# Kernel tuning notes

Hardware: AMD Instinct MI355X
Metric: run time of the kernel (lower is better)

## Reference

```python
import jax, jax.numpy as jnp
import numpy as np

N_HEADS = 16
COS_SIM_SCALE = 8.0  # lucidrains flash_cosine_sim_attention default temperature
RMS_EPS = 1e-6
ROPE_THETA = 10000.0


def _rms_norm(t, g):
    # RMSNorm over head dim with learnable gain (QKNorm)
    return t * jax.lax.rsqrt(jnp.mean(t * t, axis=-1, keepdims=True) + RMS_EPS) * g


def _rotate_half(x):
    d = x.shape[-1]
    return jnp.concatenate([-x[..., d // 2:], x[..., : d // 2]], axis=-1)


def _image_rope_cos_sin(n, d, dtype):
    # 2D axial RoPE: first half of head dim encodes row position, second half column.
    side = int(np.sqrt(n))
    assert side * side == n, 'ImageRoPE expects a square token grid'
    n_freq = d // 4
    freqs = 1.0 / (ROPE_THETA ** (jnp.arange(n_freq, dtype=jnp.float32) / n_freq))
    pos = jnp.arange(side, dtype=jnp.float32)
    grid_h = jnp.repeat(pos, side)   # (n,) row index
    grid_w = jnp.tile(pos, side)     # (n,) col index
    ang_h = grid_h[:, None] * freqs  # (n, d//4)
    ang_w = grid_w[:, None] * freqs  # (n, d//4)
    # rotate-half convention: angles for dims [0:d//2] paired with [d//2:d]
    ang = jnp.concatenate([ang_h, ang_w], axis=-1)          # (n, d//2)
    ang = jnp.concatenate([ang, ang], axis=-1)              # (n, d)
    return jnp.cos(ang).astype(dtype), jnp.sin(ang).astype(dtype)


def setup_inputs() -> dict:
    key = jax.random.key(0)
    ks = jax.random.split(key, 6)
    b, n, dm = 8, 1024, 1024
    h = N_HEADS
    d = dm // h
    s = 1.0 / np.sqrt(dm)
    return {
        'x': jax.random.normal(ks[0], (b, n, dm), dtype=jnp.float32),
        'w_qkv': jax.random.normal(ks[1], (dm, 3 * dm), dtype=jnp.float32) * s,
        'b_qkv': jnp.zeros((3 * dm,), dtype=jnp.float32),
        'q_gain': jnp.ones((d,), dtype=jnp.float32),
        'k_gain': jnp.ones((d,), dtype=jnp.float32),
        'w_out': jax.random.normal(ks[2], (dm, dm), dtype=jnp.float32) * s,
        'b_out': jnp.zeros((dm,), dtype=jnp.float32),
    }


def reference(x, w_qkv, b_qkv, q_gain, k_gain, w_out, b_out):
    b, n, dm = x.shape
    h = N_HEADS
    d = dm // h
    qkv = x @ w_qkv + b_qkv                       # (b, n, 3*dm)
    qkv = qkv.reshape(b, n, 3, h, d)
    qkv = jnp.transpose(qkv, (2, 0, 3, 1, 4))     # (3, b, h, n, d)
    q, k, v = qkv[0], qkv[1], qkv[2]
    # QK-norm (RMSNorm over head dim)
    q = _rms_norm(q, q_gain)
    k = _rms_norm(k, k_gain)
    # 2D image RoPE
    cos, sin = _image_rope_cos_sin(n, d, x.dtype)
    q = q * cos + _rotate_half(q) * sin
    k = k * cos + _rotate_half(k) * sin
    # cosine-sim attention: l2-normalize q,k, fixed scale, softmax, weighted sum
    q = q / jnp.linalg.norm(q, axis=-1, keepdims=True)
    k = k / jnp.linalg.norm(k, axis=-1, keepdims=True)
    scores = jnp.einsum('bhnd,bhmd->bhnm', q, k) * COS_SIM_SCALE
    attn = jax.nn.softmax(scores, axis=-1)
    o = jnp.einsum('bhnm,bhmd->bhnd', attn, v)    # (b, h, n, d)
    o = jnp.transpose(o, (0, 2, 1, 3)).reshape(b, n, dm)
    return o @ w_out + b_out
```

## Files before the change

### kernel.cpp

```cpp
#include <hip/hip_runtime.h>
#include <hip/hip_bf16.h>
#include <cstdint>

typedef __bf16 bf16;
typedef __bf16 bf16x8 __attribute__((ext_vector_type(8)));
typedef __bf16 bf16x4 __attribute__((ext_vector_type(4)));
typedef float f32x4 __attribute__((ext_vector_type(4)));

__device__ inline bf16x8 cvt8(const float* __restrict__ p) {
  float4 a = *(const float4*)p;
  float4 b = *(const float4*)(p + 4);
  bf16x8 r;
  r[0] = (bf16)a.x; r[1] = (bf16)a.y; r[2] = (bf16)a.z; r[3] = (bf16)a.w;
  r[4] = (bf16)b.x; r[5] = (bf16)b.y; r[6] = (bf16)b.z; r[7] = (bf16)b.w;
  return r;
}

__device__ inline void gl_lds16(const bf16* g, bf16* l) {
  auto gp = reinterpret_cast<const __attribute__((address_space(1))) uint32_t*>(
      reinterpret_cast<uintptr_t>(g));
  auto lp = reinterpret_cast<__attribute__((address_space(3))) uint32_t*>(
      reinterpret_cast<uintptr_t>(l));
  __builtin_amdgcn_global_load_lds(gp, lp, 16, 0, 0);
}

#define BAR() asm volatile("s_barrier" ::: "memory")

__global__ __launch_bounds__(256) void cast_k(const float* __restrict__ in,
                                              bf16* __restrict__ out) {
  long i = ((long)blockIdx.x * 256 + threadIdx.x) * 8;
  *(bf16x8*)(out + i) = cvt8(in + i);
}

__global__ __launch_bounds__(256) void transpose_cast_k(const float* __restrict__ in,
                                                        bf16* __restrict__ out,
                                                        int R, int C) {
  __shared__ bf16 T[32][33];
  int tc = blockIdx.x * 32, tr = blockIdx.y * 32;
  int c = threadIdx.x & 31, r8 = threadIdx.x >> 5;
#pragma unroll
  for (int i = 0; i < 4; i++) {
    int r = r8 + i * 8;
    T[r][c] = (bf16)in[(long)(tr + r) * C + tc + c];
  }
  __syncthreads();
#pragma unroll
  for (int i = 0; i < 4; i++) {
    int r = r8 + i * 8;
    out[(long)(tc + r) * R + tr + c] = T[c][r];
  }
}

__global__ __launch_bounds__(512, 2) void gemm256(const bf16* __restrict__ A,
                                                  const bf16* __restrict__ Bt,
                                                  const float* __restrict__ bias,
                                                  int K,
                                                  bf16* __restrict__ qb,
                                                  bf16* __restrict__ kb,
                                                  bf16* __restrict__ v4,
                                                  const float* __restrict__ qg,
                                                  const float* __restrict__ kg) {
  __shared__ __align__(16) bf16 As[2][16384];
  __shared__ __align__(16) bf16 Bs[2][16384];

  const int tid = threadIdx.x;
  const int lane = tid & 63;
  const int w = tid >> 6;
  const int quad = lane >> 4;
  const int l16 = lane & 15;
  const int wr = w >> 2;
  const int wc = w & 3;

  const int gx = gridDim.x;
  const int bid = blockIdx.y * gx + blockIdx.x;
  const int cpx = (gx * gridDim.y) >> 3;
  const int sw = (bid & 7) * cpx + (bid >> 3);
  const int n0 = (sw % gx) * 256;
  const int m0 = (sw / gx) * 256;

  int srow[2], scof[2];
#pragma unroll
  for (int l = 0; l < 2; l++) {
    int s = l * 512 + tid;
    srow[l] = s >> 3;
    scof[l] = ((s & 7) ^ ((s >> 3) & 7)) * 8;
  }
  const bf16* aB0 = A + (long)(m0 + srow[0]) * K + scof[0];
  const bf16* aB1 = A + (long)(m0 + srow[1]) * K + scof[1];
  const bf16* bB0 = Bt + (long)(n0 + srow[0]) * K + scof[0];
  const bf16* bB1 = Bt + (long)(n0 + srow[1]) * K + scof[1];

#define STAGE_A(tb, kt1, h)                                                        \
  {                                                                                \
    gl_lds16(aB0 + (long)(h)*128 * K + (long)(kt1)*64, &As[tb][(h)*8192 + w * 512]); \
    gl_lds16(aB1 + (long)(h)*128 * K + (long)(kt1)*64,                             \
             &As[tb][(h)*8192 + 4096 + w * 512]);                                  \
  }
#define STAGE_B(tb, kt1, h)                                                        \
  {                                                                                \
    gl_lds16(bB0 + (long)(h)*128 * K + (long)(kt1)*64, &Bs[tb][(h)*8192 + w * 512]); \
    gl_lds16(bB1 + (long)(h)*128 * K + (long)(kt1)*64,                             \
             &Bs[tb][(h)*8192 + 4096 + w * 512]);                                  \
  }

  const int cq0 = ((quad) ^ (l16 & 7)) * 8;
  const int cq1 = ((4 + quad) ^ (l16 & 7)) * 8;
  const int aoff = wr * 8192 + l16 * 64;
  const int boff = wc * 4096 + l16 * 64;

  f32x4 acc[8][4];
#pragma unroll
  for (int i = 0; i < 8; i++)
#pragma unroll
    for (int j = 0; j < 4; j++) acc[i][j] = f32x4{0.f, 0.f, 0.f, 0.f};

#define MM16(MLO, AF, BF)                                                         \
  __builtin_amdgcn_s_setprio(1);                                                  \
  _Pragma("unroll") for (int mm = 0; mm < 4; mm++)                                \
      _Pragma("unroll") for (int nn = 0; nn < 4; nn++) acc[(MLO) + mm][nn] =      \
          __builtin_amdgcn_mfma_f32_16x16x32_bf16(AF[mm], BF[nn],                 \
                                                  acc[(MLO) + mm][nn], 0, 0, 0);  \
  __builtin_amdgcn_s_setprio(0);

  const int NK = K >> 6;
  STAGE_A(0, 0, 0); STAGE_A(0, 0, 1); STAGE_B(0, 0, 0); STAGE_B(0, 0, 1);

  for (int kt = 0; kt < NK; ++kt) {
    const int pb = kt & 1;
    const int tb = pb ^ 1;
    const bool pf = (kt + 1 < NK);
    bf16x8 afr[4], bfr[4];
    if (pf) {
      STAGE_A(tb, kt + 1, 0);
      STAGE_A(tb, kt + 1, 1);
      STAGE_B(tb, kt + 1, 0);
      STAGE_B(tb, kt + 1, 1);
      asm volatile("s_waitcnt vmcnt(8)" ::: "memory");
    } else {
      asm volatile("s_waitcnt vmcnt(0)" ::: "memory");
    }
    BAR();
#pragma unroll
    for (int n = 0; n < 4; n++) bfr[n] = *(const bf16x8*)&Bs[pb][boff + n * 1024 + cq0];
#pragma unroll
    for (int m = 0; m < 4; m++) afr[m] = *(const bf16x8*)&As[pb][aoff + m * 1024 + cq0];
    MM16(0, afr, bfr)
    BAR();
#pragma unroll
    for (int m = 0; m < 4; m++)
      afr[m] = *(const bf16x8*)&As[pb][aoff + 4096 + m * 1024 + cq0];
    BAR();
    MM16(4, afr, bfr)
    BAR();
#pragma unroll
    for (int n = 0; n < 4; n++) bfr[n] = *(const bf16x8*)&Bs[pb][boff + n * 1024 + cq1];
#pragma unroll
    for (int m = 0; m < 4; m++) afr[m] = *(const bf16x8*)&As[pb][aoff + m * 1024 + cq1];
    BAR();
    MM16(0, afr, bfr)
    BAR();
#pragma unroll
    for (int m = 0; m < 4; m++)
      afr[m] = *(const bf16x8*)&As[pb][aoff + 4096 + m * 1024 + cq1];
    BAR();
    MM16(4, afr, bfr)
    BAR();
  }

  const int which = n0 >> 10;
  if (which == 2) {
    const int T0 = (((m0 & 1023) + wr * 128) >> 2) + quad;
    const int bh = (m0 >> 10) * 16 + ((n0 & 1023) >> 6) + wc;
#pragma unroll
    for (int m = 0; m < 8; m++) {
#pragma unroll
      for (int n = 0; n < 4; n++) {
        int ng = n0 + wc * 64 + n * 16 + l16;
        int dc = n * 16 + l16;
        float bj = bias[ng];
        bf16x4 pv;
#pragma unroll
        for (int r = 0; r < 4; r++) pv[r] = (bf16)(acc[m][n][r] + bj);
        *(bf16x4*)(v4 + ((long)bh * 16384 + (long)(T0 + m * 4) * 64 + dc) * 4) = pv;
      }
    }
    return;
  }

  const float* gg = which ? kg : qg;
  bf16* dst = which ? kb : qb;
  const float fold = which ? 1.0f : 8.0f;
  const int h = ((n0 + wc * 64) & 1023) >> 6;
  const int bh = (m0 >> 10) * 16 + h;
  float bj[4], gain[4];
#pragma unroll
  for (int j = 0; j < 4; j++) {
    bj[j] = bias[n0 + wc * 64 + j * 16 + l16];
    gain[j] = gg[j * 16 + l16];
  }
  const float f = exp2f((float)l16 * (-13.287712379549449f / 16.0f));

#pragma unroll
  for (int m = 0; m < 8; m++) {
#pragma unroll
    for (int r = 0; r < 4; r++) {
      int ntok = (m0 & 1023) + wr * 128 + m * 16 + quad * 4 + r;
      float v0 = acc[m][0][r] + bj[0];
      float v1 = acc[m][1][r] + bj[1];
      float v2 = acc[m][2][r] + bj[2];
      float v3 = acc[m][3][r] + bj[3];
      float ss = v0 * v0 + v1 * v1 + v2 * v2 + v3 * v3;
#pragma unroll
      for (int mk = 1; mk <= 8; mk <<= 1) ss += __shfl_xor(ss, mk, 64);
      float rms = rsqrtf(ss * (1.0f / 64.0f) + 1e-6f);
      v0 *= rms * gain[0]; v1 *= rms * gain[1]; v2 *= rms * gain[2]; v3 *= rms * gain[3];
      float sh, ch_, swv, cw;
      __sincosf((float)(ntok >> 5) * f, &sh, &ch_);
      __sincosf((float)(ntok & 31) * f, &swv, &cw);
      float w0 = v0 * ch_ - v2 * sh;
      float w1 = v1 * cw - v3 * swv;
      float w2 = v2 * ch_ + v0 * sh;
      float w3 = v3 * cw + v1 * swv;
      float nn = w0 * w0 + w1 * w1 + w2 * w2 + w3 * w3;
#pragma unroll
      for (int mk = 1; mk <= 8; mk <<= 1) nn += __shfl_xor(nn, mk, 64);
      float inv = rsqrtf(nn) * fold;
      long base = ((long)bh * 1024 + ntok) * 64 + l16;
      dst[base] = (bf16)(w0 * inv);
      dst[base + 16] = (bf16)(w1 * inv);
      dst[base + 32] = (bf16)(w2 * inv);
      dst[base + 48] = (bf16)(w3 * inv);
    }
  }
}

__global__ __launch_bounds__(256, 5) void gemm_bt1(const bf16* __restrict__ A,
                                                   const bf16* __restrict__ Bt,
                                                   const float* __restrict__ bias,
                                                   int N, int K,
                                                   float* __restrict__ out) {
  __shared__ __align__(16) bf16 As[128][32];
  __shared__ __align__(16) bf16 Bs[128][32];

  const int tid = threadIdx.x;
  const int lane = tid & 63;
  const int w = tid >> 6;
  const int wm = (w & 1) * 64;
  const int wn = (w >> 1) * 64;
  const int quad = lane >> 4;
  const int l16 = lane & 15;

  const int m0 = blockIdx.y * 128;
  const int n0 = blockIdx.x * 128;

  const int sr = w * 32 + (lane >> 2);
  const int sc = (lane & 3) * 8;

  f32x4 acc[4][4];
#pragma unroll
  for (int i = 0; i < 4; i++)
#pragma unroll
    for (int j = 0; j < 4; j++) acc[i][j] = f32x4{0.f, 0.f, 0.f, 0.f};

  for (int k0 = 0; k0 < K; k0 += 32) {
    __syncthreads();
    int hh = k0 >> 6, dc = (k0 & 63) + sc;
    int m1 = m0 + sr, m2 = m1 + 16;
    const bf16* ga0 = A + ((long)((m1 >> 10) * 16 + hh) * 1024 + (m1 & 1023)) * 64 + dc;
    const bf16* ga1 = A + ((long)((m2 >> 10) * 16 + hh) * 1024 + (m2 & 1023)) * 64 + dc;
    gl_lds16(ga0, &As[w * 32][0]);
    gl_lds16(ga1, &As[w * 32 + 16][0]);
    gl_lds16(Bt + (long)(n0 + sr) * K + k0 + sc, &Bs[w * 32][0]);
    gl_lds16(Bt + (long)(n0 + sr + 16) * K + k0 + sc, &Bs[w * 32 + 16][0]);
    __syncthreads();

    bf16x8 af[4], bfr[4];
#pragma unroll
    for (int i = 0; i < 4; i++) {
      af[i] = *(const bf16x8*)&As[wm + i * 16 + l16][quad * 8];
      bfr[i] = *(const bf16x8*)&Bs[wn + i * 16 + l16][quad * 8];
    }
#pragma unroll
    for (int i = 0; i < 4; i++)
#pragma unroll
      for (int j = 0; j < 4; j++)
        acc[i][j] = __builtin_amdgcn_mfma_f32_16x16x32_bf16(af[i], bfr[j], acc[i][j], 0, 0, 0);
  }

#pragma unroll
  for (int i = 0; i < 4; i++)
#pragma unroll
    for (int j = 0; j < 4; j++)
#pragma unroll
      for (int r = 0; r < 4; r++) {
        int mg = m0 + wm + i * 16 + quad * 4 + r;
        int ng = n0 + wn + j * 16 + l16;
        out[(long)mg * N + ng] = acc[i][j][r] + bias[ng];
      }
}

__global__ __launch_bounds__(256, 2) void attn_k(bf16* __restrict__ qb,
                                                 const bf16* __restrict__ kb,
                                                 const bf16* __restrict__ v4) {
  __shared__ __align__(16) bf16 Ks[2][64][72];
  __shared__ __align__(16) bf16 Vl[2][4096];
  __shared__ __align__(16) bf16 Ps[4][16][72];

  const int tid = threadIdx.x;
  const int lane = tid & 63;
  const int w = tid >> 6;
  const int quad = lane >> 4;
  const int l16 = lane & 15;

  const int bh = blockIdx.y;
  const int q0 = blockIdx.x * 256 + w * 64;

  bf16x8 aq[4][2];
  long qrow[4];
#pragma unroll
  for (int g = 0; g < 4; g++) {
    qrow[g] = ((long)bh * 1024 + q0 + g * 16 + l16) * 64;
    aq[g][0] = *(const bf16x8*)(qb + qrow[g] + quad * 8);
    aq[g][1] = *(const bf16x8*)(qb + qrow[g] + 32 + quad * 8);
  }

  f32x4 o[4][4];
#pragma unroll
  for (int g = 0; g < 4; g++)
#pragma unroll
    for (int i = 0; i < 4; i++) o[g][i] = f32x4{0.f, 0.f, 0.f, 0.f};
  float ls[4] = {0.f, 0.f, 0.f, 0.f};

  const int sr = tid >> 3, sc = (tid & 7) * 8;
  const bf16* kbase = kb + (long)bh * 65536;
  const bf16* vbase = v4 + (long)bh * 65536;

  bf16x8 kr0 = *(const bf16x8*)(kbase + (long)sr * 64 + sc);
  bf16x8 kr1 = *(const bf16x8*)(kbase + (long)(sr + 32) * 64 + sc);
  gl_lds16(vbase + (w * 2) * 512 + lane * 8, &Vl[0][(w * 2) * 512]);
  gl_lds16(vbase + (w * 2 + 1) * 512 + lane * 8, &Vl[0][(w * 2 + 1) * 512]);
  asm volatile("s_waitcnt vmcnt(0)" ::: "memory");
  *(bf16x8*)&Ks[0][sr][sc] = kr0;
  *(bf16x8*)&Ks[0][sr + 32][sc] = kr1;
  asm volatile("s_waitcnt lgkmcnt(0)" ::: "memory");
  BAR();

  for (int kt = 0; kt < 1024; kt += 64) {
    const int cur = (kt >> 6) & 1;
    const bool pf = (kt + 64 < 1024);
    if (pf) {
      kr0 = *(const bf16x8*)(kbase + (long)(kt + 64 + sr) * 64 + sc);
      kr1 = *(const bf16x8*)(kbase + (long)(kt + 64 + sr + 32) * 64 + sc);
      gl_lds16(vbase + (long)(kt + 64) * 64 + (w * 2) * 512 + lane * 8,
               &Vl[cur ^ 1][(w * 2) * 512]);
      gl_lds16(vbase + (long)(kt + 64) * 64 + (w * 2 + 1) * 512 + lane * 8,
               &Vl[cur ^ 1][(w * 2 + 1) * 512]);
    }

    bf16x8 kf[4][2], vf[4][2];
#pragma unroll
    for (int i = 0; i < 4; i++) {
      kf[i][0] = *(const bf16x8*)&Ks[cur][i * 16 + l16][quad * 8];
      kf[i][1] = *(const bf16x8*)&Ks[cur][i * 16 + l16][32 + quad * 8];
      int D4 = (i * 16 + l16) * 4;
      bf16x4 a0 = *(const bf16x4*)&Vl[cur][quad * 512 + D4];
      bf16x4 a1 = *(const bf16x4*)&Vl[cur][quad * 512 + D4 + 256];
      bf16x4 a2 = *(const bf16x4*)&Vl[cur][quad * 512 + D4 + 2048];
      bf16x4 a3 = *(const bf16x4*)&Vl[cur][quad * 512 + D4 + 2048 + 256];
      vf[i][0] = __builtin_shufflevector(a0, a1, 0, 1, 2, 3, 4, 5, 6, 7);
      vf[i][1] = __builtin_shufflevector(a2, a3, 0, 1, 2, 3, 4, 5, 6, 7);
    }

#pragma unroll
    for (int g = 0; g < 4; g++) {
#pragma unroll
      for (int i = 0; i < 4; i++) {
        f32x4 st = f32x4{0.f, 0.f, 0.f, 0.f};
        st = __builtin_amdgcn_mfma_f32_16x16x32_bf16(kf[i][0], aq[g][0], st, 0, 0, 0);
        st = __builtin_amdgcn_mfma_f32_16x16x32_bf16(kf[i][1], aq[g][1], st, 0, 0, 0);
        bf16x4 pk;
#pragma unroll
        for (int r = 0; r < 4; r++) {
          float p = __expf(st[r] - 8.0f);
          ls[g] += p;
          pk[r] = (bf16)p;
        }
        *(bf16x4*)&Ps[w][l16][i * 16 + quad * 4] = pk;
      }
      asm volatile("s_waitcnt lgkmcnt(0)" ::: "memory");
      bf16x8 bp0 = *(const bf16x8*)&Ps[w][l16][quad * 8];
      bf16x8 bp1 = *(const bf16x8*)&Ps[w][l16][32 + quad * 8];
#pragma unroll
      for (int i = 0; i < 4; i++) {
        o[g][i] = __builtin_amdgcn_mfma_f32_16x16x32_bf16(vf[i][0], bp0, o[g][i], 0, 0, 0);
        o[g][i] = __builtin_amdgcn_mfma_f32_16x16x32_bf16(vf[i][1], bp1, o[g][i], 0, 0, 0);
      }
    }

    if (pf) {
      asm volatile("s_waitcnt vmcnt(0)" ::: "memory");
      *(bf16x8*)&Ks[cur ^ 1][sr][sc] = kr0;
      *(bf16x8*)&Ks[cur ^ 1][sr + 32][sc] = kr1;
    }
    asm volatile("s_waitcnt lgkmcnt(0)" ::: "memory");
    BAR();
  }

#pragma unroll
  for (int g = 0; g < 4; g++) {
    float l = ls[g];
    l += __shfl_xor(l, 16, 64);
    l += __shfl_xor(l, 32, 64);
    float inv = 1.0f / l;
#pragma unroll
    for (int i = 0; i < 4; i++) {
      bf16x4 ov;
#pragma unroll
      for (int r = 0; r < 4; r++) ov[r] = (bf16)(o[g][i][r] * inv);
      *(bf16x4*)(qb + qrow[g] + i * 16 + quad * 4) = ov;
    }
  }
}

extern "C" void kernel_launch(void* const* d_in, const int* in_sizes, int n_in,
                              void* d_out, int out_size, void* d_ws, size_t ws_size,
                              hipStream_t stream) {
  (void)in_sizes; (void)n_in; (void)out_size; (void)ws_size;
  const float* x     = (const float*)d_in[0];
  const float* w_qkv = (const float*)d_in[1];
  const float* b_qkv = (const float*)d_in[2];
  const float* q_g   = (const float*)d_in[3];
  const float* k_g   = (const float*)d_in[4];
  const float* w_out = (const float*)d_in[5];
  const float* b_out = (const float*)d_in[6];
  float* out = (float*)d_out;

  char* ws = (char*)d_ws;
  bf16* wqkvT = (bf16*)ws; ws += (long)3072 * 1024 * 2;
  bf16* woT   = (bf16*)ws; ws += (long)1024 * 1024 * 2;
  bf16* xb    = (bf16*)ws; ws += (long)8192 * 1024 * 2;
  bf16* qb    = (bf16*)ws; ws += (long)128 * 1024 * 64 * 2;
  bf16* kb    = (bf16*)ws; ws += (long)128 * 1024 * 64 * 2;
  bf16* v4    = (bf16*)ws; ws += (long)128 * 64 * 1024 * 2;

  cast_k<<<4096, 256, 0, stream>>>(x, xb);
  transpose_cast_k<<<dim3(3072 / 32, 1024 / 32), 256, 0, stream>>>(w_qkv, wqkvT, 1024, 3072);
  transpose_cast_k<<<dim3(1024 / 32, 1024 / 32), 256, 0, stream>>>(w_out, woT, 1024, 1024);
  gemm256<<<dim3(3072 / 256, 8192 / 256), 512, 0, stream>>>(xb, wqkvT, b_qkv, 1024,
                                                            qb, kb, v4, q_g, k_g);
  attn_k<<<dim3(4, 128), 256, 0, stream>>>(qb, kb, v4);
  gemm_bt1<<<dim3(1024 / 128, 8192 / 128), 256, 0, stream>>>(qb, woT, b_out,
                                                             1024, 1024, out);
}
```

Baseline: 266.5 us.

## Shrink QKV GEMM tile to 128x256 with K-step 32 for higher occupancy

```diff
diff --git a/kernel.cpp b/kernel.cpp
--- a/kernel.cpp
+++ b/kernel.cpp
@@ -51,7 +51,7 @@
   }
 }
 
-__global__ __launch_bounds__(512, 2) void gemm256(const bf16* __restrict__ A,
+__global__ __launch_bounds__(512, 4) void gemm256(const bf16* __restrict__ A,
                                                   const bf16* __restrict__ Bt,
                                                   const float* __restrict__ bias,
                                                   int K,
@@ -60,8 +60,8 @@
                                                   bf16* __restrict__ v4,
                                                   const float* __restrict__ qg,
                                                   const float* __restrict__ kg) {
-  __shared__ __align__(16) bf16 As[2][16384];
-  __shared__ __align__(16) bf16 Bs[2][16384];
+  __shared__ __align__(16) bf16 As[2][4096];
+  __shared__ __align__(16) bf16 Bs[2][8192];
 
   const int tid = threadIdx.x;
   const int lane = tid & 63;
@@ -76,103 +76,67 @@
   const int cpx = (gx * gridDim.y) >> 3;
   const int sw = (bid & 7) * cpx + (bid >> 3);
   const int n0 = (sw % gx) * 256;
-  const int m0 = (sw / gx) * 256;
-
-  int srow[2], scof[2];
-#pragma unroll
-  for (int l = 0; l < 2; l++) {
-    int s = l * 512 + tid;
-    srow[l] = s >> 3;
-    scof[l] = ((s & 7) ^ ((s >> 3) & 7)) * 8;
-  }
-  const bf16* aB0 = A + (long)(m0 + srow[0]) * K + scof[0];
-  const bf16* aB1 = A + (long)(m0 + srow[1]) * K + scof[1];
-  const bf16* bB0 = Bt + (long)(n0 + srow[0]) * K + scof[0];
-  const bf16* bB1 = Bt + (long)(n0 + srow[1]) * K + scof[1];
-
-#define STAGE_A(tb, kt1, h)                                                        \
-  {                                                                                \
-    gl_lds16(aB0 + (long)(h)*128 * K + (long)(kt1)*64, &As[tb][(h)*8192 + w * 512]); \
-    gl_lds16(aB1 + (long)(h)*128 * K + (long)(kt1)*64,                             \
-             &As[tb][(h)*8192 + 4096 + w * 512]);                                  \
-  }
-#define STAGE_B(tb, kt1, h)                                                        \
-  {                                                                                \
-    gl_lds16(bB0 + (long)(h)*128 * K + (long)(kt1)*64, &Bs[tb][(h)*8192 + w * 512]); \
-    gl_lds16(bB1 + (long)(h)*128 * K + (long)(kt1)*64,                             \
-             &Bs[tb][(h)*8192 + 4096 + w * 512]);                                  \
-  }
-
-  const int cq0 = ((quad) ^ (l16 & 7)) * 8;
-  const int cq1 = ((4 + quad) ^ (l16 & 7)) * 8;
-  const int aoff = wr * 8192 + l16 * 64;
-  const int boff = wc * 4096 + l16 * 64;
-
-  f32x4 acc[8][4];
-#pragma unroll
-  for (int i = 0; i < 8; i++)
+  const int m0 = (sw / gx) * 128;
+
+  const int srA = tid >> 2;
+  const int scS = ((tid & 3) ^ ((tid >> 3) & 3)) * 8;
+  const bf16* aS = A + (long)(m0 + srA) * K + scS;
+  const bf16* bS0 = Bt + (long)(n0 + srA) * K + scS;
+  const bf16* bS1 = bS0 + (long)128 * K;
+
+#define STAGE(tb, kt1)                                                   \
+  {                                                                      \
+    const long kc = (long)(kt1)*32;                                      \
+    gl_lds16(aS + kc, &As[tb][w * 512]);                                 \
+    gl_lds16(bS0 + kc, &Bs[tb][w * 512]);                                \
+    gl_lds16(bS1 + kc, &Bs[tb][4096 + w * 512]);                         \
+  }
+
+  const int cphys = (quad ^ ((l16 >> 1) & 3)) * 8;
+  const int aoff = (wr * 64 + l16) * 32 + cphys;
+  const int boff = (wc * 64 + l16) * 32 + cphys;
+
+  f32x4 acc[4][4];
+#pragma unroll
+  for (int i = 0; i < 4; i++)
 #pragma unroll
     for (int j = 0; j < 4; j++) acc[i][j] = f32x4{0.f, 0.f, 0.f, 0.f};
 
-#define MM16(MLO, AF, BF)                                                         \
-  __builtin_amdgcn_s_setprio(1);                                                  \
-  _Pragma("unroll") for (int mm = 0; mm < 4; mm++)                                \
-      _Pragma("unroll") for (int nn = 0; nn < 4; nn++) acc[(MLO) + mm][nn] =      \
-          __builtin_amdgcn_mfma_f32_16x16x32_bf16(AF[mm], BF[nn],                 \
-                                                  acc[(MLO) + mm][nn], 0, 0, 0);  \
-  __builtin_amdgcn_s_setprio(0);
-
-  const int NK = K >> 6;
-  STAGE_A(0, 0, 0); STAGE_A(0, 0, 1); STAGE_B(0, 0, 0); STAGE_B(0, 0, 1);
+  const int NK = K >> 5;
+  STAGE(0, 0);
 
   for (int kt = 0; kt < NK; ++kt) {
     const int pb = kt & 1;
     const int tb = pb ^ 1;
     const bool pf = (kt + 1 < NK);
-    bf16x8 afr[4], bfr[4];
     if (pf) {
-      STAGE_A(tb, kt + 1, 0);
-      STAGE_A(tb, kt + 1, 1);
-      STAGE_B(tb, kt + 1, 0);
-      STAGE_B(tb, kt + 1, 1);
-      asm volatile("s_waitcnt vmcnt(8)" ::: "memory");
+      STAGE(tb, kt + 1);
+      asm volatile("s_waitcnt vmcnt(3)" ::: "memory");
     } else {
       asm volatile("s_waitcnt vmcnt(0)" ::: "memory");
     }
     BAR();
-#pragma unroll
-    for (int n = 0; n < 4; n++) bfr[n] = *(const bf16x8*)&Bs[pb][boff + n * 1024 + cq0];
-#pragma unroll
-    for (int m = 0; m < 4; m++) afr[m] = *(const bf16x8*)&As[pb][aoff + m * 1024 + cq0];
-    MM16(0, afr, bfr)
-    BAR();
+    bf16x8 afr[4], bfr[4];
+#pragma unroll
+    for (int n = 0; n < 4; n++) bfr[n] = *(const bf16x8*)&Bs[pb][boff + n * 512];
+#pragma unroll
+    for (int m = 0; m < 4; m++) afr[m] = *(const bf16x8*)&As[pb][aoff + m * 512];
+    __builtin_amdgcn_s_setprio(1);
 #pragma unroll
     for (int m = 0; m < 4; m++)
-      afr[m] = *(const bf16x8*)&As[pb][aoff + 4096 + m * 1024 + cq0];
-    BAR();
-    MM16(4, afr, bfr)
-    BAR();
-#pragma unroll
-    for (int n = 0; n < 4; n++) bfr[n] = *(const bf16x8*)&Bs[pb][boff + n * 1024 + cq1];
-#pragma unroll
-    for (int m = 0; m < 4; m++) afr[m] = *(const bf16x8*)&As[pb][aoff + m * 1024 + cq1];
-    BAR();
-    MM16(0, afr, bfr)
-    BAR();
-#pragma unroll
-    for (int m = 0; m < 4; m++)
-      afr[m] = *(const bf16x8*)&As[pb][aoff + 4096 + m * 1024 + cq1];
-    BAR();
-    MM16(4, afr, bfr)
+#pragma unroll
+      for (int n = 0; n < 4; n++)
+        acc[m][n] = __builtin_amdgcn_mfma_f32_16x16x32_bf16(afr[m], bfr[n], acc[m][n], 0, 0, 0);
+    __builtin_amdgcn_s_setprio(0);
     BAR();
   }
 
   const int which = n0 >> 10;
   if (which == 2) {
-    const int T0 = (((m0 & 1023) + wr * 128) >> 2) + quad;
-    const int bh = (m0 >> 10) * 16 + ((n0 & 1023) >> 6) + wc;
-#pragma unroll
-    for (int m = 0; m < 8; m++) {
+    const int T0 = (((m0 & 1023) + wr * 64) >> 2) + quad;
+    const int bh = (m0 >> 10) * 16 + (((n0 + wc * 64) & 1023) >> 6);
+#pragma unroll
+    for (int m = 0; m < 4; m++) {
 #pragma unroll
       for (int n = 0; n < 4; n++) {
         int ng = n0 + wc * 64 + n * 16 + l16;
@@ -201,10 +165,10 @@
   const float f = exp2f((float)l16 * (-13.287712379549449f / 16.0f));
 
 #pragma unroll
-  for (int m = 0; m < 8; m++) {
+  for (int m = 0; m < 4; m++) {
 #pragma unroll
     for (int r = 0; r < 4; r++) {
-      int ntok = (m0 & 1023) + wr * 128 + m * 16 + quad * 4 + r;
+      int ntok = (m0 & 1023) + wr * 64 + m * 16 + quad * 4 + r;
       float v0 = acc[m][0][r] + bj[0];
       float v1 = acc[m][1][r] + bj[1];
       float v2 = acc[m][2][r] + bj[2];
@@ -446,7 +410,7 @@
   cast_k<<<4096, 256, 0, stream>>>(x, xb);
   transpose_cast_k<<<dim3(3072 / 32, 1024 / 32), 256, 0, stream>>>(w_qkv, wqkvT, 1024, 3072);
   transpose_cast_k<<<dim3(1024 / 32, 1024 / 32), 256, 0, stream>>>(w_out, woT, 1024, 1024);
-  gemm256<<<dim3(3072 / 256, 8192 / 256), 512, 0, stream>>>(xb, wqkvT, b_qkv, 1024,
+  gemm256<<<dim3(3072 / 256, 8192 / 128), 512, 0, stream>>>(xb, wqkvT, b_qkv, 1024,
                                                             qb, kb, v4, q_g, k_g);
   attn_k<<<dim3(4, 128), 256, 0, stream>>>(qb, kb, v4);
   gemm_bt1<<<dim3(1024 / 128, 8192 / 128), 256, 0, stream>>>(qb, woT, b_out,
```

Result: no change. 261.7 us (-1.8%).
